# Kernel tuning notes

Measured on AMD Instinct MI355X. Metric: run time of the kernel, lower is better.

Reference implementation:

```python
import jax, jax.numpy as jnp
import numpy as np

D_MODEL = 2048
N_HEAD = 16
D_HEAD = D_MODEL // N_HEAD


def setup_inputs() -> dict:
    key = jax.random.key(0)
    k_x, k_qkv, k_proj = jax.random.split(key, 3)
    x = jax.random.normal(k_x, (2, 2048, D_MODEL), dtype=jnp.float32)
    # nn.Linear weights: out = x @ W.T ; store as [out, in] like torch
    scale = 1.0 / np.sqrt(D_MODEL)
    W_qkv = jax.random.uniform(k_qkv, (3 * D_MODEL, D_MODEL), jnp.float32, -scale, scale)
    W_proj = jax.random.uniform(k_proj, (D_MODEL, D_MODEL), jnp.float32, -scale, scale)
    return {"x": x, "W_qkv": W_qkv, "W_proj": W_proj}


def reference(x, W_qkv, W_proj):
    B, T, C = x.shape
    qkv = jnp.einsum('btc,oc->bto', x, W_qkv)  # [B,T,3C]
    q, k, v = jnp.split(qkv, 3, axis=-1)
    def heads(t):
        return t.reshape(B, T, N_HEAD, D_HEAD).transpose(0, 2, 1, 3)  # [B,H,T,Dh]
    q, k, v = heads(q), heads(k), heads(v)
    att = jnp.einsum('bhqd,bhkd->bhqk', q, k) / jnp.sqrt(jnp.float32(D_HEAD))
    causal = jnp.tril(jnp.ones((T, T), dtype=bool))  # True = keep
    att = jnp.where(causal, att, -jnp.inf)
    att = jax.nn.softmax(att, axis=-1)
    y = jnp.einsum('bhqk,bhkd->bhqd', att, v)
    y = y.transpose(0, 2, 1, 3).reshape(B, T, C)
    return jnp.einsum('btc,oc->bto', y, W_proj)
```

## Files before the change

kernel.cpp:

```cpp
#include <hip/hip_runtime.h>
#include <hip/hip_bf16.h>
#include <stdint.h>


typedef __bf16 bf16x8 __attribute__((ext_vector_type(8)));
typedef float f32x4 __attribute__((ext_vector_type(4)));
typedef unsigned short u16x8 __attribute__((ext_vector_type(8)));
typedef unsigned short u16x4 __attribute__((ext_vector_type(4)));

__device__ __forceinline__ unsigned short f2bf(float f) {
  unsigned int u = __builtin_bit_cast(unsigned int, f);
  u += 0x7fff + ((u >> 16) & 1);
  return (unsigned short)(u >> 16);
}
__device__ __forceinline__ float bf2f(unsigned short u) {
  return __builtin_bit_cast(float, (unsigned int)u << 16);
}

__device__ __forceinline__ u16x8 cvt8(const float* p) {
  f32x4 lo = *(const f32x4*)p;
  f32x4 hi = *(const f32x4*)(p + 4);
  u16x8 r;
#pragma unroll
  for (int j = 0; j < 4; j++) { r[j] = f2bf(lo[j]); r[4 + j] = f2bf(hi[j]); }
  return r;
}

__device__ __forceinline__ void gload16(const void* g, void* l) {
  __builtin_amdgcn_global_load_lds(
      (const __attribute__((address_space(1))) void*)g,
      (__attribute__((address_space(3))) void*)l, 16, 0, 0);
}

__global__ __launch_bounds__(256) void f32_to_bf16(
    const float* __restrict__ src, unsigned short* __restrict__ dst, int n8) {
  int i = blockIdx.x * 256 + threadIdx.x;
  const int stride = gridDim.x * 256;
  for (; i < n8; i += stride) {
    u16x8 v = cvt8(src + (size_t)i * 8);
    *(u16x8*)&dst[(size_t)i * 8] = v;
  }
}

template <bool COF32>
__global__ __launch_bounds__(256) void gemm_bf(
    const unsigned short* __restrict__ A, const unsigned short* __restrict__ B,
    void* __restrict__ Cv, int M, int N, int K) {
  __shared__ __align__(16) unsigned short Alds[128 * 32];
  __shared__ __align__(16) unsigned short Blds[128 * 32];

  const int tid  = threadIdx.x;
  const int lane = tid & 63;
  const int w    = tid >> 6;
  const int ln   = lane & 15;
  const int kq   = lane >> 4;
  const int m0 = blockIdx.y * 128;
  const int n0 = blockIdx.x * 128;
  const int m_base = (w >> 1) * 64;
  const int n_base = (w & 1) * 64;

  f32x4 acc[4][4];
#pragma unroll
  for (int i = 0; i < 4; i++)
#pragma unroll
    for (int j = 0; j < 4; j++) acc[i][j] = {0.f, 0.f, 0.f, 0.f};

  const int c0 = tid;
  const int c1 = tid + 256;
  const unsigned short* Ag0 = A + (size_t)(m0 + (c0 >> 2)) * K + (c0 & 3) * 8;
  const unsigned short* Ag1 = A + (size_t)(m0 + (c1 >> 2)) * K + (c1 & 3) * 8;
  const unsigned short* Bg0 = B + (size_t)(n0 + (c0 >> 2)) * K + (c0 & 3) * 8;
  const unsigned short* Bg1 = B + (size_t)(n0 + (c1 >> 2)) * K + (c1 & 3) * 8;
  unsigned short* lA0 = &Alds[(size_t)w * 512];
  unsigned short* lA1 = &Alds[2048 + (size_t)w * 512];
  unsigned short* lB0 = &Blds[(size_t)w * 512];
  unsigned short* lB1 = &Blds[2048 + (size_t)w * 512];

  const int nk = K >> 5;
  for (int kt = 0; kt < nk; kt++) {
    const int ko = kt * 32;
    gload16(Ag0 + ko, lA0);
    gload16(Ag1 + ko, lA1);
    gload16(Bg0 + ko, lB0);
    gload16(Bg1 + ko, lB1);
    __syncthreads();

    bf16x8 af[4], bfr[4];
#pragma unroll
    for (int i = 0; i < 4; i++)
      af[i] = *(const bf16x8*)&Alds[(m_base + i * 16 + ln) * 32 + kq * 8];
#pragma unroll
    for (int j = 0; j < 4; j++)
      bfr[j] = *(const bf16x8*)&Blds[(n_base + j * 16 + ln) * 32 + kq * 8];
#pragma unroll
    for (int i = 0; i < 4; i++)
#pragma unroll
      for (int j = 0; j < 4; j++)
        acc[i][j] = __builtin_amdgcn_mfma_f32_16x16x32_bf16(af[i], bfr[j], acc[i][j], 0, 0, 0);
    __syncthreads();
  }

#pragma unroll
  for (int i = 0; i < 4; i++) {
    const int row_base = m0 + m_base + i * 16 + kq * 4;
#pragma unroll
    for (int j = 0; j < 4; j++) {
      const int col = n0 + n_base + j * 16 + ln;
#pragma unroll
      for (int r = 0; r < 4; r++) {
        const size_t idx = (size_t)(row_base + r) * N + col;
        if (COF32) ((float*)Cv)[idx] = acc[i][j][r];
        else       ((unsigned short*)Cv)[idx] = f2bf(acc[i][j][r]);
      }
    }
  }
}

#define TSEQ 2048
#define CDIM 2048
#define QKVLD 6144
#define DH 128
#define NEG_BIG (-1.0e30f)
#define K_LD 136
#define VT_LD 76
#define P_LD 72

__global__ __launch_bounds__(256) void attn(
    const unsigned short* __restrict__ qkv,
    unsigned short* __restrict__ y) {
  __shared__ __align__(16) unsigned short Klds[64 * K_LD];
  __shared__ __align__(16) unsigned short Vt[DH * VT_LD];
  __shared__ __align__(16) unsigned short Plds[4 * 16 * P_LD];

  const int tid  = threadIdx.x;
  const int lane = tid & 63;
  const int w    = tid >> 6;
  const int ln   = lane & 15;
  const int kq   = lane >> 4;
  const int qt = blockIdx.x;
  const int h  = blockIdx.y;
  const int b  = blockIdx.z;
  const int q0 = qt * 64;
  const int qrow = q0 + w * 16 + ln;

  const size_t baseQ = (size_t)b * TSEQ * QKVLD + (size_t)h * DH;
  const size_t baseK = baseQ + CDIM;
  const size_t baseV = baseQ + 2 * CDIM;

  bf16x8 qf[4];
  {
    const float scale = 0.08838834764831845f;
    const unsigned short* qp = qkv + baseQ + (size_t)qrow * QKVLD + kq * 8;
#pragma unroll
    for (int kc = 0; kc < 4; kc++) {
      u16x8 raw = *(const u16x8*)(qp + kc * 32);
      u16x8 t;
#pragma unroll
      for (int j = 0; j < 8; j++) t[j] = f2bf(bf2f(raw[j]) * scale);
      qf[kc] = __builtin_bit_cast(bf16x8, t);
    }
  }

  const int kRow = tid >> 4;
  const int kCol = (tid & 15) * 8;
  const int vK4  = (tid & 15) * 4;
  const int vD0  = (tid >> 4) * 8;
  const unsigned short* Kg = qkv + baseK + (size_t)kRow * QKVLD + kCol;
  const unsigned short* Vg = qkv + baseV + (size_t)vK4 * QKVLD + vD0;

  u16x8 kreg[4], vreg[4];
#pragma unroll
  for (int it = 0; it < 4; it++)
    kreg[it] = *(const u16x8*)(Kg + (size_t)(it * 16) * QKVLD);
#pragma unroll
  for (int r = 0; r < 4; r++)
    vreg[r] = *(const u16x8*)(Vg + (size_t)r * QKVLD);

  f32x4 o[8];
#pragma unroll
  for (int i = 0; i < 8; i++) o[i] = {0.f, 0.f, 0.f, 0.f};
  float m = NEG_BIG, l = 0.f;
  unsigned short* pw = &Plds[w * 16 * P_LD];

  for (int kt = 0; kt <= qt; kt++) {
    __syncthreads();

#pragma unroll
    for (int it = 0; it < 4; it++)
      *(u16x8*)&Klds[(kRow + it * 16) * K_LD + kCol] = kreg[it];
#pragma unroll
    for (int j = 0; j < 8; j++) {
      u16x4 t = {vreg[0][j], vreg[1][j], vreg[2][j], vreg[3][j]};
      *(u16x4*)&Vt[(vD0 + j) * VT_LD + vK4] = t;
    }
    __syncthreads();

    if (kt < qt) {
      const size_t off = (size_t)(kt + 1) * 64 * QKVLD;
#pragma unroll
      for (int it = 0; it < 4; it++)
        kreg[it] = *(const u16x8*)(Kg + off + (size_t)(it * 16) * QKVLD);
#pragma unroll
      for (int r = 0; r < 4; r++)
        vreg[r] = *(const u16x8*)(Vg + off + (size_t)r * QKVLD);
    }

    f32x4 s[4];
#pragma unroll
    for (int nt = 0; nt < 4; nt++) {
      s[nt] = {0.f, 0.f, 0.f, 0.f};
#pragma unroll
      for (int kc = 0; kc < 4; kc++) {
        bf16x8 kb = *(const bf16x8*)&Klds[(nt * 16 + ln) * K_LD + kc * 32 + kq * 8];
        s[nt] = __builtin_amdgcn_mfma_f32_16x16x32_bf16(kb, qf[kc], s[nt], 0, 0, 0);
      }
    }

    if (kt == qt) {
      const int kbase = kt * 64 + kq * 4;
#pragma unroll
      for (int nt = 0; nt < 4; nt++)
#pragma unroll
        for (int r = 0; r < 4; r++)
          if (kbase + nt * 16 + r > qrow) s[nt][r] = NEG_BIG;
    }

    float mt;
    {
      f32x4 t01 = {fmaxf(s[0][0], s[0][1]), fmaxf(s[0][2], s[0][3]),
                   fmaxf(s[1][0], s[1][1]), fmaxf(s[1][2], s[1][3])};
      f32x4 t23 = {fmaxf(s[2][0], s[2][1]), fmaxf(s[2][2], s[2][3]),
                   fmaxf(s[3][0], s[3][1]), fmaxf(s[3][2], s[3][3])};
      f32x4 t = {fmaxf(t01[0], t01[1]), fmaxf(t01[2], t01[3]),
                 fmaxf(t23[0], t23[1]), fmaxf(t23[2], t23[3])};
      mt = fmaxf(fmaxf(t[0], t[1]), fmaxf(t[2], t[3]));
    }
    mt = fmaxf(mt, __shfl_xor(mt, 16, 64));
    mt = fmaxf(mt, __shfl_xor(mt, 32, 64));
    const float mn = fmaxf(m, mt);
    const float alpha = __expf(m - mn);
    m = mn;

    float ps = 0.f;
#pragma unroll
    for (int nt = 0; nt < 4; nt++) {
      u16x4 pbits;
#pragma unroll
      for (int r = 0; r < 4; r++) {
        const float p = __expf(s[nt][r] - mn);
        ps += p;
        pbits[r] = f2bf(p);
      }
      *(u16x4*)&pw[ln * P_LD + nt * 16 + kq * 4] = pbits;
    }
    ps += __shfl_xor(ps, 16, 64);
    ps += __shfl_xor(ps, 32, 64);
    l = l * alpha + ps;

#pragma unroll
    for (int i = 0; i < 8; i++)
#pragma unroll
      for (int r = 0; r < 4; r++) o[i][r] *= alpha;

    bf16x8 pa[2];
#pragma unroll
    for (int kc = 0; kc < 2; kc++)
      pa[kc] = *(const bf16x8*)&pw[ln * P_LD + kc * 32 + kq * 8];
#pragma unroll
    for (int nt = 0; nt < 8; nt++)
#pragma unroll
      for (int kc = 0; kc < 2; kc++) {
        bf16x8 vb = *(const bf16x8*)&Vt[(nt * 16 + ln) * VT_LD + kc * 32 + kq * 8];
        o[nt] = __builtin_amdgcn_mfma_f32_16x16x32_bf16(vb, pa[kc], o[nt], 0, 0, 0);
      }
  }

  const float inv = 1.f / l;
  unsigned short* yp = y + (size_t)(b * TSEQ + qrow) * CDIM + (size_t)h * DH + kq * 4;
#pragma unroll
  for (int nt = 0; nt < 8; nt++) {
    u16x4 ov;
#pragma unroll
    for (int r = 0; r < 4; r++) ov[r] = f2bf(o[nt][r] * inv);
    *(u16x4*)(yp + nt * 16) = ov;
  }
}

extern "C" void kernel_launch(void* const* d_in, const int* in_sizes, int n_in,
                              void* d_out, int out_size, void* d_ws, size_t ws_size,
                              hipStream_t stream) {
  const float* x     = (const float*)d_in[0];
  const float* Wqkv  = (const float*)d_in[1];
  const float* Wproj = (const float*)d_in[2];
  void* out = d_out;

  unsigned short* qkv = (unsigned short*)d_ws;
  unsigned short* y   = qkv + (size_t)4096 * 6144;
  unsigned short* xbf = y;
  unsigned short* wbf = y + (size_t)4096 * 2048;

  f32_to_bf16<<<dim3(2048), 256, 0, stream>>>(x, xbf, (4096 * 2048) / 8);
  f32_to_bf16<<<dim3(2048), 256, 0, stream>>>(Wqkv, wbf, (6144 * 2048) / 8);
  gemm_bf<false><<<dim3(48, 32), 256, 0, stream>>>(xbf, wbf, qkv, 4096, 6144, 2048);
  f32_to_bf16<<<dim3(2048), 256, 0, stream>>>(Wproj, wbf, (2048 * 2048) / 8);
  attn<<<dim3(32, 16, 2), 256, 0, stream>>>(qkv, y);
  gemm_bf<true><<<dim3(16, 32), 256, 0, stream>>>(y, wbf, out, 4096, 2048, 2048);
}
```

Measured before the change: 461.6 us.

## Use 128-row query blocks with 8 waves, reversed scheduling and lazy rescale

The attention kernel now runs 512-thread blocks covering 128 query rows. Each K/V tile loaded into LDS is shared by 8 waves instead of 4, which halves global K/V traffic per query. Blocks are linearised so that the heaviest causal blocks of batch 0 launch first for load balance. The online-softmax max update and the rescale of the output accumulator are skipped when the new tile max exceeds the running max by at most 8, which saves exp and multiply work. In exchange, waves past their causal limit sit idle while still joining the barriers, and the unrescaled exponentials can grow up to e^8 before normalisation.

```diff
diff --git a/kernel.cpp b/kernel.cpp
--- a/kernel.cpp
+++ b/kernel.cpp
@@ -125,22 +125,26 @@
 #define VT_LD 76
 #define P_LD 72
 
-__global__ __launch_bounds__(256) void attn(
+__global__ __launch_bounds__(512, 4) void attn(
     const unsigned short* __restrict__ qkv,
     unsigned short* __restrict__ y) {
   __shared__ __align__(16) unsigned short Klds[64 * K_LD];
   __shared__ __align__(16) unsigned short Vt[DH * VT_LD];
-  __shared__ __align__(16) unsigned short Plds[4 * 16 * P_LD];
+  __shared__ __align__(16) unsigned short Plds[8 * 16 * P_LD];
 
   const int tid  = threadIdx.x;
   const int lane = tid & 63;
   const int w    = tid >> 6;
   const int ln   = lane & 15;
   const int kq   = lane >> 4;
-  const int qt = blockIdx.x;
-  const int h  = blockIdx.y;
-  const int b  = blockIdx.z;
-  const int q0 = qt * 64;
+
+  const int idx  = blockIdx.x;
+  const int half = idx >> 8;
+  const int qbi  = idx & 15;
+  const int qb   = half ? qbi : 15 - qbi;
+  const int h    = (idx >> 4) & 15;
+  const int b    = half;
+  const int q0   = qb * 128;
   const int qrow = q0 + w * 16 + ln;
 
   const size_t baseQ = (size_t)b * TSEQ * QKVLD + (size_t)h * DH;
@@ -164,17 +168,18 @@
   const int kRow = tid >> 4;
   const int kCol = (tid & 15) * 8;
   const int vK4  = (tid & 15) * 4;
-  const int vD0  = (tid >> 4) * 8;
+  const int vD0  = (tid >> 4) * 4;
   const unsigned short* Kg = qkv + baseK + (size_t)kRow * QKVLD + kCol;
   const unsigned short* Vg = qkv + baseV + (size_t)vK4 * QKVLD + vD0;
 
-  u16x8 kreg[4], vreg[4];
-#pragma unroll
-  for (int it = 0; it < 4; it++)
-    kreg[it] = *(const u16x8*)(Kg + (size_t)(it * 16) * QKVLD);
+  u16x8 kreg[2];
+  u16x4 vreg[4];
+#pragma unroll
+  for (int it = 0; it < 2; it++)
+    kreg[it] = *(const u16x8*)(Kg + (size_t)(it * 32) * QKVLD);
 #pragma unroll
   for (int r = 0; r < 4; r++)
-    vreg[r] = *(const u16x8*)(Vg + (size_t)r * QKVLD);
+    vreg[r] = *(const u16x4*)(Vg + (size_t)r * QKVLD);
 
   f32x4 o[8];
 #pragma unroll
@@ -182,28 +187,33 @@
   float m = NEG_BIG, l = 0.f;
   unsigned short* pw = &Plds[w * 16 * P_LD];
 
-  for (int kt = 0; kt <= qt; kt++) {
+  const int ktEnd   = 2 * qb + 2;
+  const int myKtMax = (q0 + w * 16) >> 6;
+
+  for (int kt = 0; kt < ktEnd; kt++) {
     __syncthreads();
 
 #pragma unroll
-    for (int it = 0; it < 4; it++)
-      *(u16x8*)&Klds[(kRow + it * 16) * K_LD + kCol] = kreg[it];
-#pragma unroll
-    for (int j = 0; j < 8; j++) {
+    for (int it = 0; it < 2; it++)
+      *(u16x8*)&Klds[(kRow + it * 32) * K_LD + kCol] = kreg[it];
+#pragma unroll
+    for (int j = 0; j < 4; j++) {
       u16x4 t = {vreg[0][j], vreg[1][j], vreg[2][j], vreg[3][j]};
       *(u16x4*)&Vt[(vD0 + j) * VT_LD + vK4] = t;
     }
     __syncthreads();
 
-    if (kt < qt) {
+    if (kt + 1 < ktEnd) {
       const size_t off = (size_t)(kt + 1) * 64 * QKVLD;
 #pragma unroll
-      for (int it = 0; it < 4; it++)
-        kreg[it] = *(const u16x8*)(Kg + off + (size_t)(it * 16) * QKVLD);
+      for (int it = 0; it < 2; it++)
+        kreg[it] = *(const u16x8*)(Kg + off + (size_t)(it * 32) * QKVLD);
 #pragma unroll
       for (int r = 0; r < 4; r++)
-        vreg[r] = *(const u16x8*)(Vg + off + (size_t)r * QKVLD);
-    }
+        vreg[r] = *(const u16x4*)(Vg + off + (size_t)r * QKVLD);
+    }
+
+    if (kt > myKtMax) continue;
 
     f32x4 s[4];
 #pragma unroll
@@ -216,7 +226,7 @@
       }
     }
 
-    if (kt == qt) {
+    if (kt == myKtMax) {
       const int kbase = kt * 64 + kq * 4;
 #pragma unroll
       for (int nt = 0; nt < 4; nt++)
@@ -237,8 +247,10 @@
     }
     mt = fmaxf(mt, __shfl_xor(mt, 16, 64));
     mt = fmaxf(mt, __shfl_xor(mt, 32, 64));
-    const float mn = fmaxf(m, mt);
-    const float alpha = __expf(m - mn);
+
+    const bool defer = __all(mt - m <= 8.0f);
+    const float mn = defer ? m : fmaxf(m, mt);
+    const float alpha = defer ? 1.0f : __expf(m - mn);
     m = mn;
 
     float ps = 0.f;
@@ -257,10 +269,12 @@
     ps += __shfl_xor(ps, 32, 64);
     l = l * alpha + ps;
 
-#pragma unroll
-    for (int i = 0; i < 8; i++)
-#pragma unroll
-      for (int r = 0; r < 4; r++) o[i][r] *= alpha;
+    if (!defer) {
+#pragma unroll
+      for (int i = 0; i < 8; i++)
+#pragma unroll
+        for (int r = 0; r < 4; r++) o[i][r] *= alpha;
+    }
 
     bf16x8 pa[2];
 #pragma unroll
@@ -303,6 +317,6 @@
   f32_to_bf16<<<dim3(2048), 256, 0, stream>>>(Wqkv, wbf, (6144 * 2048) / 8);
   gemm_bf<false><<<dim3(48, 32), 256, 0, stream>>>(xbf, wbf, qkv, 4096, 6144, 2048);
   f32_to_bf16<<<dim3(2048), 256, 0, stream>>>(Wproj, wbf, (2048 * 2048) / 8);
-  attn<<<dim3(32, 16, 2), 256, 0, stream>>>(qkv, y);
+  attn<<<dim3(512), 512, 0, stream>>>(qkv, y);
   gemm_bf<true><<<dim3(16, 32), 256, 0, stream>>>(y, wbf, out, 4096, 2048, 2048);
 }
```

Result: faster. 393.4 us (-14.8%).
